# Optimization experiments

Hardware: AMD Instinct MI355X
Metric: run time of the kernel (lower is better)

## Reference

```python
import jax, jax.numpy as jnp
import numpy as np

B, IN, OUT = 384, 512, 384  # B must equal OUT (broadcast in original sigma_3 + diag(sigma_bias))


def setup_inputs() -> dict:
    key = jax.random.key(0)
    k1, k2, k3, k4 = jax.random.split(key, 4)
    mu = jax.random.normal(k1, (B, IN), dtype=jnp.float32)
    sigma = jax.random.uniform(k2, (B, IN, IN), dtype=jnp.float32)
    # nn.Linear weight: normal(0, 0.1); bias filled with 1e-4
    W = 0.1 * jax.random.normal(k3, (OUT, IN), dtype=jnp.float32)
    b = jnp.full((OUT,), 1e-4, dtype=jnp.float32)
    # sigma_weight ~ U(-12, -2.2); sigma_bias = ones * bias(True)
    sigma_weight = jax.random.uniform(k4, (OUT, IN), minval=-12.0, maxval=-2.2, dtype=jnp.float32)
    sigma_bias = jnp.ones((OUT,), dtype=jnp.float32)
    return {"mu": mu, "sigma": sigma, "W": W, "b": b,
            "sigma_weight": sigma_weight, "sigma_bias": sigma_bias}


def reference(mu, sigma, W, b, sigma_weight, sigma_bias):
    sp = jnp.log1p(jnp.exp(sigma_weight))            # softplus(sigma_weight), [OUT, IN]
    mu_f = mu @ W.T + b                              # [B, OUT]
    # sigma_1: diag( sum_i sigma[b,i,i] * sp[o,i] )  (equivalent to the torch
    # diag_embed / batched-matmul / diagonal chain, without the [B,OUT,IN,IN] blowup)
    diag_sigma = jnp.diagonal(sigma, axis1=1, axis2=2)   # [B, IN]
    s1 = jnp.einsum('bi,oi->bo', diag_sigma, sp)         # [B, OUT]
    # sigma_2 = W @ sigma @ W^T, dense part
    s2 = jnp.einsum('oi,bij,pj->bop', W, sigma, W)       # [B, OUT, OUT]
    # sigma_3 = sp @ mu^2 + diag(sigma_bias)  ([B,OUT] + [OUT,OUT], valid since B==OUT)
    s3 = jnp.square(mu) @ sp.T + jnp.diag(sigma_bias)    # [B, OUT]
    eye = jnp.eye(sp.shape[0], dtype=mu.dtype)
    sigma_out = (s1 + s3)[:, :, None] * eye + s2         # [B, OUT, OUT]
    return mu_f, sigma_out
```

## Files before the change

### kernel.cpp

```cpp
#include <hip/hip_runtime.h>
#include <hip/hip_bf16.h>
#include <math.h>

#define Bn   384
#define INn  512
#define OUTn 384

typedef __bf16 bf16x8 __attribute__((ext_vector_type(8)));
typedef __bf16 bf16x4 __attribute__((ext_vector_type(4)));
typedef float  f32x4  __attribute__((ext_vector_type(4)));

__device__ __bf16 g_Wf [OUTn * INn];
__device__ float  g_Wt [INn * OUTn];
__device__ float  g_spt[INn * OUTn];
__device__ float  g_d  [Bn * OUTn];
__device__ float  g_t  [Bn * INn];
__device__ __bf16 g_U  [(size_t)Bn * OUTn * INn];

__global__ __launch_bounds__(256) void prep_kernel(const float* __restrict__ W,
                                                   const float* __restrict__ sw) {
    int idx = blockIdx.x * 256 + threadIdx.x;
    if (idx < OUTn * INn) {
        const int o = idx >> 9, i = idx & 511;
        float w = W[idx];
        const int f = ((((o >> 4) * 16 + (i >> 5)) * 4 + ((i >> 3) & 3)) * 16 + (o & 15)) * 8 + (i & 7);
        g_Wf[f] = (__bf16)w;
        g_Wt[i * OUTn + o] = w;
        float x = sw[idx];
        g_spt[i * OUTn + o] = (x > 20.f) ? x : log1pf(expf(x));
    }
}

__global__ __launch_bounds__(512, 4) void passA_kernel(const float* __restrict__ sigma) {
    __shared__ __align__(16) unsigned char smem[49152];
    typedef __bf16 AsT[64][136];
    AsT* As = (AsT*)smem;

    const int it   = blockIdx.x;
    const int b    = blockIdx.y;
    const int tid  = threadIdx.x;
    const int wave = tid >> 6, lane = tid & 63;
    const int quad = lane >> 4, l15 = lane & 15;
    const int i0     = it * 64;
    const int p_base = wave * 48;
    const int srow   = tid >> 3;
    const int scol   = (tid & 7) * 16;

    const float* sigb   = sigma + (size_t)b * (INn * INn);
    const float* srcRow = sigb + (size_t)(i0 + srow) * INn + scol;

    float4 r0, r1, r2, r3;

    auto LOAD = [&](int c) {
        const float4* p = (const float4*)(srcRow + c * 128);
        r0 = p[0]; r1 = p[1]; r2 = p[2]; r3 = p[3];
    };
    auto STORE = [&](int c, int buf) {
        const int ig   = i0 + srow;
        const int base = c * 128 + scol;
        if (ig >= base && ig < base + 16) {
            const int j = ig - base;
            float4 v = (j < 4) ? r0 : (j < 8) ? r1 : (j < 12) ? r2 : r3;
            const int e = j & 3;
            float dv = (e == 0) ? v.x : (e == 1) ? v.y : (e == 2) ? v.z : v.w;
            g_t[b * INn + ig] = dv;
        }
        bf16x8 t0, t1;
        t0[0]=(__bf16)r0.x; t0[1]=(__bf16)r0.y; t0[2]=(__bf16)r0.z; t0[3]=(__bf16)r0.w;
        t0[4]=(__bf16)r1.x; t0[5]=(__bf16)r1.y; t0[6]=(__bf16)r1.z; t0[7]=(__bf16)r1.w;
        t1[0]=(__bf16)r2.x; t1[1]=(__bf16)r2.y; t1[2]=(__bf16)r2.z; t1[3]=(__bf16)r2.w;
        t1[4]=(__bf16)r3.x; t1[5]=(__bf16)r3.y; t1[6]=(__bf16)r3.z; t1[7]=(__bf16)r3.w;
        *(bf16x8*)&As[buf][srow][scol]     = t0;
        *(bf16x8*)&As[buf][srow][scol + 8] = t1;
    };

    f32x4 acc[4][3];
#pragma unroll
    for (int mi = 0; mi < 4; ++mi)
#pragma unroll
        for (int nf = 0; nf < 3; ++nf) acc[mi][nf] = (f32x4){0.f, 0.f, 0.f, 0.f};

    auto COMPUTE = [&](int buf, int kc0) {
#pragma unroll
        for (int kcl = 0; kcl < 128; kcl += 32) {
            bf16x8 afr[4];
#pragma unroll
            for (int mi = 0; mi < 4; ++mi)
                afr[mi] = *(const bf16x8*)&As[buf][mi * 16 + l15][kcl + quad * 8];
#pragma unroll
            for (int nf = 0; nf < 3; ++nf) {
                const int ot   = wave * 3 + nf;
                const int kc32 = (kc0 + kcl) >> 5;
                const __bf16* bp = g_Wf + ((((size_t)(ot * 16 + kc32) * 4 + quad) * 16 + l15) << 3);
                bf16x8 bfr = *(const bf16x8*)bp;
#pragma unroll
                for (int mi = 0; mi < 4; ++mi)
                    acc[mi][nf] = __builtin_amdgcn_mfma_f32_16x16x32_bf16(afr[mi], bfr, acc[mi][nf], 0, 0, 0);
            }
        }
    };

    LOAD(0); STORE(0, 0); LOAD(1);
    __syncthreads();
    COMPUTE(0, 0);
    __syncthreads(); STORE(1, 1); LOAD(2); __syncthreads();
    COMPUTE(1, 128);
    __syncthreads(); STORE(2, 0); LOAD(3); __syncthreads();
    COMPUTE(0, 256);
    __syncthreads(); STORE(3, 1); __syncthreads();
    COMPUTE(1, 384);

    __syncthreads();
    __bf16* Uo = (__bf16*)smem;
#pragma unroll
    for (int mi = 0; mi < 4; ++mi) {
        const int i4l = mi * 4 + quad;
#pragma unroll
        for (int nf = 0; nf < 3; ++nf) {
            const int p = p_base + nf * 16 + l15;
            bf16x4 v;
            v[0] = (__bf16)acc[mi][nf][0];
            v[1] = (__bf16)acc[mi][nf][1];
            v[2] = (__bf16)acc[mi][nf][2];
            v[3] = (__bf16)acc[mi][nf][3];
            *(bf16x4*)&Uo[(i4l * OUTn + p) * 4] = v;
        }
    }
    __syncthreads();
    {
        char* dst = (char*)(g_U + (size_t)(b * 128 + it * 16) * 1536);
#pragma unroll
        for (int r = 0; r < 6; ++r) {
            const int L = r * 8192 + tid * 16;
            *(bf16x8*)(dst + L) = *(const bf16x8*)(smem + L);
        }
    }
}

__global__ __launch_bounds__(384) void k2_kernel(const float* __restrict__ mu,
                                                 const float* __restrict__ bias,
                                                 const float* __restrict__ sbias,
                                                 float* __restrict__ out_muf) {
    const int b = blockIdx.x;
    const int t = threadIdx.x;
    __shared__ __align__(16) float muL[INn];
    __shared__ __align__(16) float tL[INn];
    for (int i = t; i < INn; i += 384) {
        float m = mu[b * INn + i];
        muL[i] = m;
        tL[i] = g_t[b * INn + i] + m * m;
    }
    __syncthreads();
    float mf = 0.f, dd = 0.f;
#pragma unroll 8
    for (int i = 0; i < INn; ++i) {
        mf += g_Wt[i * OUTn + t] * muL[i];
        dd += g_spt[i * OUTn + t] * tL[i];
    }
    out_muf[b * OUTn + t] = mf + bias[t];
    g_d[b * OUTn + t] = dd + (t == b ? sbias[t] : 0.f);
}

__global__ __launch_bounds__(512, 4) void passB_kernel(float* __restrict__ outS) {
    __shared__ __align__(16) float Os[192 * 64];

    const int ptile = blockIdx.x;
    const int b     = blockIdx.y;
    const int tid   = threadIdx.x;
    const int wave  = tid >> 6, lane = tid & 63;
    const int quad  = lane >> 4, l15 = lane & 15;
    const int p0     = ptile * 64;
    const int o_base = wave * 48;

    const __bf16* Ub = g_U + (size_t)b * (OUTn * INn);

    f32x4 acc[3][4];
#pragma unroll
    for (int mi = 0; mi < 3; ++mi)
#pragma unroll
        for (int nf = 0; nf < 4; ++nf) acc[mi][nf] = (f32x4){0.f, 0.f, 0.f, 0.f};

    for (int kc = 0; kc < INn; kc += 32) {
        bf16x8 afr[3];
#pragma unroll
        for (int mi = 0; mi < 3; ++mi) {
            const int ot = wave * 3 + mi;
            const __bf16* ap = g_Wf + ((((size_t)(ot * 16 + (kc >> 5)) * 4 + quad) * 16 + l15) << 3);
            afr[mi] = *(const bf16x8*)ap;
        }
        const int i4 = (kc >> 2) + quad * 2;
#pragma unroll
        for (int nf = 0; nf < 4; ++nf) {
            const int p = p0 + nf * 16 + l15;
            bf16x4 lo = *(const bf16x4*)(Ub + ((size_t)i4 * OUTn + p) * 4);
            bf16x4 hi = *(const bf16x4*)(Ub + ((size_t)(i4 + 1) * OUTn + p) * 4);
            bf16x8 bfr;
            bfr[0]=lo[0]; bfr[1]=lo[1]; bfr[2]=lo[2]; bfr[3]=lo[3];
            bfr[4]=hi[0]; bfr[5]=hi[1]; bfr[6]=hi[2]; bfr[7]=hi[3];
#pragma unroll
            for (int mi = 0; mi < 3; ++mi)
                acc[mi][nf] = __builtin_amdgcn_mfma_f32_16x16x32_bf16(afr[mi], bfr, acc[mi][nf], 0, 0, 0);
        }
    }

    float* outb = outS + (size_t)b * (OUTn * OUTn);
    const int halfId = wave >> 2;
#pragma unroll
    for (int h = 0; h < 2; ++h) {
        if (h) __syncthreads();
        if (halfId == h) {
#pragma unroll
            for (int mi = 0; mi < 3; ++mi) {
                const int o_loc = (wave & 3) * 48 + mi * 16 + quad * 4;
#pragma unroll
                for (int nf = 0; nf < 4; ++nf) {
                    const int p_loc = nf * 16 + l15;
                    const int p = p0 + p_loc;
#pragma unroll
                    for (int r = 0; r < 4; ++r) {
                        const int o = h * 192 + o_loc + r;
                        float v = acc[mi][nf][r];
                        if (o == p) v += g_d[b * OUTn + o];
                        Os[(o_loc + r) * 64 + p_loc] = v;
                    }
                }
            }
        }
        __syncthreads();
#pragma unroll
        for (int r = 0; r < 6; ++r) {
            const int L     = r * 8192 + tid * 16;
            const int o_loc = L >> 8;
            const int pb    = L & 255;
            *(f32x4*)((char*)outb + (size_t)(h * 192 + o_loc) * (OUTn * 4) + p0 * 4 + pb) =
                *(const f32x4*)((const char*)Os + L);
        }
    }
}

extern "C" void kernel_launch(void* const* d_in, const int* in_sizes, int n_in,
                              void* d_out, int out_size, void* d_ws, size_t ws_size,
                              hipStream_t stream) {
    const float* mu    = (const float*)d_in[0];
    const float* sigma = (const float*)d_in[1];
    const float* W     = (const float*)d_in[2];
    const float* bias  = (const float*)d_in[3];
    const float* sw    = (const float*)d_in[4];
    const float* sbias = (const float*)d_in[5];

    float* out     = (float*)d_out;
    float* out_muf = out;
    float* out_sig = out + Bn * OUTn;

    prep_kernel<<<(OUTn * INn + 255) / 256, 256, 0, stream>>>(W, sw);
    passA_kernel<<<dim3(8, Bn), 512, 0, stream>>>(sigma);
    k2_kernel<<<Bn, 384, 0, stream>>>(mu, bias, sbias, out_muf);
    passB_kernel<<<dim3(6, Bn), 512, 0, stream>>>(out_sig);
}
```

Before: 1.010 ms.

## Stream sigma tiles into LDS with async global_load_lds and double buffering

passA now copies fp32 sigma tiles straight from global memory into a swizzled LDS layout using global_load_lds. The old path staged them through registers and converted them to bf16 before storing. The K loop becomes eight double-buffered 64-wide chunks, with the next chunk's copy issued before the current chunk's MFMAs. Conversion to bf16 moves to fragment-read time, and the diagonal extraction now reads from the swizzled LDS tile. The aim is to cut register staging and VALU work and overlap the dominant sigma read with compute. The cost is double the LDS bytes per element, per-fragment conversion work, and reliance on correct wait handling for the async copies.

```diff
diff --git a/kernel.cpp b/kernel.cpp
--- a/kernel.cpp
+++ b/kernel.cpp
@@ -33,7 +33,7 @@
 
 __global__ __launch_bounds__(512, 4) void passA_kernel(const float* __restrict__ sigma) {
     __shared__ __align__(16) unsigned char smem[49152];
-    typedef __bf16 AsT[64][136];
+    typedef float AsT[64][64];
     AsT* As = (AsT*)smem;
 
     const int it   = blockIdx.x;
@@ -43,74 +43,70 @@
     const int quad = lane >> 4, l15 = lane & 15;
     const int i0     = it * 64;
     const int p_base = wave * 48;
-    const int srow   = tid >> 3;
-    const int scol   = (tid & 7) * 16;
-
-    const float* sigb   = sigma + (size_t)b * (INn * INn);
-    const float* srcRow = sigb + (size_t)(i0 + srow) * INn + scol;
-
-    float4 r0, r1, r2, r3;
-
-    auto LOAD = [&](int c) {
-        const float4* p = (const float4*)(srcRow + c * 128);
-        r0 = p[0]; r1 = p[1]; r2 = p[2]; r3 = p[3];
+
+    const float* sigb = sigma + (size_t)b * (INn * INn);
+
+    auto STAGE = [&](int c, int buf) {
+#pragma unroll
+        for (int g = 0; g < 2; ++g) {
+            const int rt  = wave * 8 + g * 4 + (lane >> 4);
+            const int g16 = (lane & 15) ^ (rt & 15);
+            const float* src = sigb + (size_t)(i0 + rt) * INn + c * 64 + g16 * 4;
+            float* dst = &As[buf][wave * 8 + g * 4][0];
+            __builtin_amdgcn_global_load_lds(
+                (const __attribute__((address_space(1))) void*)src,
+                (__attribute__((address_space(3))) void*)dst, 16, 0, 0);
+        }
     };
-    auto STORE = [&](int c, int buf) {
-        const int ig   = i0 + srow;
-        const int base = c * 128 + scol;
-        if (ig >= base && ig < base + 16) {
-            const int j = ig - base;
-            float4 v = (j < 4) ? r0 : (j < 8) ? r1 : (j < 12) ? r2 : r3;
-            const int e = j & 3;
-            float dv = (e == 0) ? v.x : (e == 1) ? v.y : (e == 2) ? v.z : v.w;
-            g_t[b * INn + ig] = dv;
-        }
-        bf16x8 t0, t1;
-        t0[0]=(__bf16)r0.x; t0[1]=(__bf16)r0.y; t0[2]=(__bf16)r0.z; t0[3]=(__bf16)r0.w;
-        t0[4]=(__bf16)r1.x; t0[5]=(__bf16)r1.y; t0[6]=(__bf16)r1.z; t0[7]=(__bf16)r1.w;
-        t1[0]=(__bf16)r2.x; t1[1]=(__bf16)r2.y; t1[2]=(__bf16)r2.z; t1[3]=(__bf16)r2.w;
-        t1[4]=(__bf16)r3.x; t1[5]=(__bf16)r3.y; t1[6]=(__bf16)r3.z; t1[7]=(__bf16)r3.w;
-        *(bf16x8*)&As[buf][srow][scol]     = t0;
-        *(bf16x8*)&As[buf][srow][scol + 8] = t1;
+
+    f32x4 acc[4][3];
+#pragma unroll
+    for (int mi = 0; mi < 4; ++mi)
+#pragma unroll
+        for (int nf = 0; nf < 3; ++nf) acc[mi][nf] = (f32x4){0.f, 0.f, 0.f, 0.f};
+
+    auto COMPUTE = [&](int buf, int c) {
+#pragma unroll
+        for (int ks = 0; ks < 2; ++ks) {
+            const int kc32 = c * 2 + ks;
+            bf16x8 bfr[3];
+#pragma unroll
+            for (int nf = 0; nf < 3; ++nf) {
+                const int ot = wave * 3 + nf;
+                bfr[nf] = *(const bf16x8*)(g_Wf +
+                    ((((size_t)(ot * 16 + kc32) * 4 + quad) * 16 + l15) << 3));
+            }
+#pragma unroll
+            for (int mi = 0; mi < 4; ++mi) {
+                const int rt = mi * 16 + l15;
+                const int e  = ks * 8 + quad * 2;
+                f32x4 x0 = *(const f32x4*)&As[buf][rt][(e ^ l15) * 4];
+                f32x4 x1 = *(const f32x4*)&As[buf][rt][((e + 1) ^ l15) * 4];
+                bf16x8 a;
+                a[0]=(__bf16)x0[0]; a[1]=(__bf16)x0[1]; a[2]=(__bf16)x0[2]; a[3]=(__bf16)x0[3];
+                a[4]=(__bf16)x1[0]; a[5]=(__bf16)x1[1]; a[6]=(__bf16)x1[2]; a[7]=(__bf16)x1[3];
+#pragma unroll
+                for (int nf = 0; nf < 3; ++nf)
+                    acc[mi][nf] = __builtin_amdgcn_mfma_f32_16x16x32_bf16(a, bfr[nf], acc[mi][nf], 0, 0, 0);
+            }
+        }
     };
 
-    f32x4 acc[4][3];
-#pragma unroll
-    for (int mi = 0; mi < 4; ++mi)
-#pragma unroll
-        for (int nf = 0; nf < 3; ++nf) acc[mi][nf] = (f32x4){0.f, 0.f, 0.f, 0.f};
-
-    auto COMPUTE = [&](int buf, int kc0) {
-#pragma unroll
-        for (int kcl = 0; kcl < 128; kcl += 32) {
-            bf16x8 afr[4];
-#pragma unroll
-            for (int mi = 0; mi < 4; ++mi)
-                afr[mi] = *(const bf16x8*)&As[buf][mi * 16 + l15][kcl + quad * 8];
-#pragma unroll
-            for (int nf = 0; nf < 3; ++nf) {
-                const int ot   = wave * 3 + nf;
-                const int kc32 = (kc0 + kcl) >> 5;
-                const __bf16* bp = g_Wf + ((((size_t)(ot * 16 + kc32) * 4 + quad) * 16 + l15) << 3);
-                bf16x8 bfr = *(const bf16x8*)bp;
-#pragma unroll
-                for (int mi = 0; mi < 4; ++mi)
-                    acc[mi][nf] = __builtin_amdgcn_mfma_f32_16x16x32_bf16(afr[mi], bfr, acc[mi][nf], 0, 0, 0);
-            }
-        }
-    };
-
-    LOAD(0); STORE(0, 0); LOAD(1);
+    STAGE(0, 0);
     __syncthreads();
-    COMPUTE(0, 0);
-    __syncthreads(); STORE(1, 1); LOAD(2); __syncthreads();
-    COMPUTE(1, 128);
-    __syncthreads(); STORE(2, 0); LOAD(3); __syncthreads();
-    COMPUTE(0, 256);
-    __syncthreads(); STORE(3, 1); __syncthreads();
-    COMPUTE(1, 384);
-
-    __syncthreads();
+    int buf = 0;
+#pragma unroll
+    for (int c = 0; c < 8; ++c) {
+        if (c < 7) STAGE(c + 1, buf ^ 1);
+        COMPUTE(buf, c);
+        if (c == it && tid < 64) {
+            const int u = (tid >> 2) ^ (tid & 15);
+            g_t[b * INn + i0 + tid] = As[buf][tid][u * 4 + (tid & 3)];
+        }
+        __syncthreads();
+        buf ^= 1;
+    }
+
     __bf16* Uo = (__bf16*)smem;
 #pragma unroll
     for (int mi = 0; mi < 4; ++mi) {
@@ -170,7 +166,6 @@
     const int wave  = tid >> 6, lane = tid & 63;
     const int quad  = lane >> 4, l15 = lane & 15;
     const int p0     = ptile * 64;
-    const int o_base = wave * 48;
 
     const __bf16* Ub = g_U + (size_t)b * (OUTn * INn);
 
```

Result: faster. 841.5 us (-16.6%).
